# Kernel tuning notes

Hardware: AMD Instinct MI355X
Metric: run time of the kernel (lower is better)

## Reference

```python
import jax, jax.numpy as jnp
import numpy as np

G, N, D, L, T = 64, 64, 128, 4, 10
SLOPE = 0.01
BN_EPS = 1e-5


def _gin(x, adj, mask, W1, b1, W2, b2, eps):
    # x: [B,N,D], adj: [B,N,N], mask: [B,N] bool
    agg = jnp.einsum('bnm,bmd->bnd', adj, x)
    h = (1.0 + eps) * x + agg
    h = jax.nn.leaky_relu(h @ W1 + b1, SLOPE)
    h = h @ W2 + b2
    return h * mask[..., None].astype(h.dtype)


def _masked_bn(h, mask, gamma, beta):
    # training-mode BatchNorm1d over the masked (valid) rows only
    m = mask[..., None].astype(h.dtype)
    cnt = jnp.sum(m)
    mean = jnp.sum(h * m, axis=(0, 1)) / cnt
    var = jnp.sum(((h - mean) ** 2) * m, axis=(0, 1)) / cnt  # biased, as BN
    hn = (h - mean) * jax.lax.rsqrt(var + BN_EPS) * gamma + beta
    return jnp.where(mask[..., None], hn, h)


def _seg_mean(v, idx, num_segments):
    s = jax.ops.segment_sum(v, idx, num_segments=num_segments)
    c = jax.ops.segment_sum(jnp.ones((v.shape[0],), v.dtype), idx, num_segments=num_segments)
    return s / jnp.maximum(c, 1.0).reshape((num_segments,) + (1,) * (v.ndim - 1))


def setup_inputs() -> dict:
    key = jax.random.key(0)
    ks = jax.random.split(key, 16)
    S = G * N
    # original graphs: symmetric binary adjacency, no self loops
    a = (jax.random.uniform(ks[0], (G, N, N)) > 0.9).astype(jnp.float32)
    a = jnp.triu(a, 1)
    original_adj = a + a.transpose(0, 2, 1)
    original_mask = jnp.ones((G, N), dtype=bool)
    # node-deleted policy: subgraph s of graph s//N deletes node s%N
    graph_idx = jnp.repeat(jnp.arange(G), N)
    deleted = jnp.tile(jnp.arange(N), G)
    mask = jnp.ones((S, N), dtype=bool).at[jnp.arange(S), deleted].set(False)
    mf = mask.astype(jnp.float32)
    adj = original_adj[graph_idx] * mf[:, :, None] * mf[:, None, :]
    x = jax.random.normal(ks[1], (S, N, D), dtype=jnp.float32)
    sc = 1.0 / np.sqrt(D)
    inp = dict(
        x=x, adj=adj, original_adj=original_adj,
        gnn_W1=jax.random.normal(ks[2], (L, D, D)) * sc,
        gnn_b1=jnp.zeros((L, D)),
        gnn_W2=jax.random.normal(ks[3], (L, D, D)) * sc,
        gnn_b2=jnp.zeros((L, D)),
        gnn_eps=jnp.zeros((L,)),
        gs_W1=jax.random.normal(ks[4], (L, D, D)) * sc,
        gs_b1=jnp.zeros((L, D)),
        gs_W2=jax.random.normal(ks[5], (L, D, D)) * sc,
        gs_b2=jnp.zeros((L, D)),
        gs_eps=jnp.zeros((L,)),
        bn_gamma=jnp.ones((L, D)), bn_beta=jnp.zeros((L, D)),
        bns_gamma=jnp.ones((L, D)), bns_beta=jnp.zeros((L, D)),
        fin_W1=jax.random.normal(ks[6], (D, 2 * D)) * sc,
        fin_b1=jnp.zeros((2 * D,)),
        fin_W2=jax.random.normal(ks[7], (2 * D, T)) * (1.0 / np.sqrt(2 * D)),
        fin_b2=jnp.zeros((T,)),
        mask=mask, original_mask=original_mask, graph_idx=graph_idx,
    )
    return inp


def reference(x, adj, original_adj, gnn_W1, gnn_b1, gnn_W2, gnn_b2, gnn_eps,
              gs_W1, gs_b1, gs_W2, gs_b2, gs_eps,
              bn_gamma, bn_beta, bns_gamma, bns_beta,
              fin_W1, fin_b1, fin_W2, fin_b2,
              mask, original_mask, graph_idx):
    for i in range(L):
        h1 = _gin(x, adj, mask, gnn_W1[i], gnn_b1[i], gnn_W2[i], gnn_b2[i], gnn_eps[i])
        h1 = _masked_bn(h1, mask, bn_gamma[i], bn_beta[i])
        x_sum = _seg_mean(x, graph_idx, G)  # [G,N,D] scatter-mean over subgraphs
        h2 = _gin(x_sum, original_adj, original_mask, gs_W1[i], gs_b1[i], gs_W2[i], gs_b2[i], gs_eps[i])
        h2 = _masked_bn(h2, original_mask, bns_gamma[i], bns_beta[i])
        x = jax.nn.leaky_relu(h1 + h2[graph_idx], SLOPE)
    num_nodes = jnp.sum(mask, axis=-1).astype(x.dtype)  # [S]
    h_sub = jnp.sum(x, axis=1) / num_nodes[:, None]     # mean pool per subgraph
    h_graph = _seg_mean(h_sub, graph_idx, G)            # [G,D]
    out = jax.nn.leaky_relu(h_graph @ fin_W1 + fin_b1, SLOPE) @ fin_W2 + fin_b2
    return out
```

## Files before the change

### kernel.cpp

```cpp
#include <hip/hip_runtime.h>
#include <hip/hip_bf16.h>


typedef __bf16 bf16x8 __attribute__((ext_vector_type(8)));
typedef float f32x4 __attribute__((ext_vector_type(4)));
typedef unsigned short us8 __attribute__((ext_vector_type(8)));
typedef unsigned short us4 __attribute__((ext_vector_type(4)));
typedef unsigned u32x4 __attribute__((ext_vector_type(4)));
typedef unsigned u32x2 __attribute__((ext_vector_type(2)));

__device__ __forceinline__ unsigned short f2b(float f) {
  unsigned u = __builtin_bit_cast(unsigned, f);
  u += 0x7FFFu + ((u >> 16) & 1u);
  return (unsigned short)(u >> 16);
}
__device__ __forceinline__ unsigned cvtpk(float lo, float hi) {
  unsigned r;
  asm("v_cvt_pk_bf16_f32 %0, %1, %2" : "=v"(r) : "v"(lo), "v"(hi));
  return r;
}
__device__ __forceinline__ float b2f(unsigned short h) {
  return __builtin_bit_cast(float, (unsigned)h << 16);
}
__device__ __forceinline__ f32x4 mm(bf16x8 a, bf16x8 b, f32x4 c) {
  return __builtin_amdgcn_mfma_f32_16x16x32_bf16(a, b, c, 0, 0, 0);
}
__device__ __forceinline__ bf16x8 frag(const char* base, int row, int Kelems, int k0) {
  int off = (row * Kelems + k0) * 2;
  off ^= (row & 7) << 4;
  return *(const bf16x8*)(base + off);
}
__device__ __forceinline__ float lk(float v) { return fmaxf(v, 0.01f * v); }

__global__ __launch_bounds__(256) void k_prep(const float* __restrict__ g1,
    const float* __restrict__ g2, const float* __restrict__ s1,
    const float* __restrict__ s2, unsigned short* __restrict__ wt) {
  int b = blockIdx.x;
  int l = b >> 2, j = b & 3;
  const float* src = (j == 0 ? g1 : j == 1 ? g2 : j == 2 ? s1 : s2) + l * 16384;
  unsigned short* dst = wt + b * 16384;
  for (int e = threadIdx.x; e < 16384; e += 256) {
    int n = e >> 7, k = e & 127;
    dst[e] = f2b(src[k * 128 + n]);
  }
}

__global__ __launch_bounds__(256) void k_pack(const float* __restrict__ adj,
    const float* __restrict__ oadj, unsigned short* __restrict__ badj,
    unsigned short* __restrict__ boadj) {
  int bid = blockIdx.x, t = threadIdx.x;
  bool SUB = bid < 4096;
  int sub = SUB ? bid : bid - 4096;
  const float* src = SUB ? adj : oadj;
  unsigned short* dst = SUB ? badj : boadj;
  const float* p = src + (size_t)sub * 4096 + (t >> 2) * 64 + (t & 3) * 16;
  unsigned bits = 0;
  #pragma unroll
  for (int j4 = 0; j4 < 4; ++j4) {
    float4 v = *(const float4*)(p + j4 * 4);
    bits |= (unsigned)(v.x != 0.f) << (j4 * 4);
    bits |= (unsigned)(v.y != 0.f) << (j4 * 4 + 1);
    bits |= (unsigned)(v.z != 0.f) << (j4 * 4 + 2);
    bits |= (unsigned)(v.w != 0.f) << (j4 * 4 + 3);
  }
  dst[(size_t)sub * 256 + t] = (unsigned short)bits;
}

__global__ __launch_bounds__(256) void k_castseg(const float* __restrict__ x,
    unsigned short* __restrict__ xw, float* __restrict__ pxs) {
  int b2 = blockIdx.x, bb = b2 >> 2, c = b2 & 3, t = threadIdx.x;
  int e0 = c * 2048 + t * 8;
  float acc[8];
  #pragma unroll
  for (int j = 0; j < 8; ++j) acc[j] = 0.f;
  for (int ss = 0; ss < 16; ++ss) {
    size_t sb = ((size_t)bb * 16 + ss) * 8192 + e0;
    float4 v0 = *(const float4*)(x + sb);
    float4 v1 = *(const float4*)(x + sb + 4);
    acc[0] += v0.x; acc[1] += v0.y; acc[2] += v0.z; acc[3] += v0.w;
    acc[4] += v1.x; acc[5] += v1.y; acc[6] += v1.z; acc[7] += v1.w;
    u32x4 pk;
    pk.x = cvtpk(v0.x, v0.y); pk.y = cvtpk(v0.z, v0.w);
    pk.z = cvtpk(v1.x, v1.y); pk.w = cvtpk(v1.z, v1.w);
    *(us8*)(xw + sb) = __builtin_bit_cast(us8, pk);
  }
  float* o = pxs + (size_t)bb * 8192 + e0;
  *(float4*)o = make_float4(acc[0], acc[1], acc[2], acc[3]);
  *(float4*)(o + 4) = make_float4(acc[4], acc[5], acc[6], acc[7]);
}

template<int LAST>
__global__ __launch_bounds__(256) void k_xpart(const unsigned short* __restrict__ h1T,
    const unsigned short* __restrict__ h2T, const float* __restrict__ bnA,
    const float* __restrict__ bnB, const float* __restrict__ bnsA,
    const float* __restrict__ bnsB, float* __restrict__ pxsT,
    float* __restrict__ ppool) {
  int b2 = blockIdx.x, bb = b2 >> 2, c = b2 & 3, g = bb >> 2;
  int t = threadIdx.x;
  int d = c * 32 + (t >> 3), n0 = (t & 7) * 8;
  size_t off = (size_t)d * 64 + n0;
  float A1 = bnA[d], B1 = bnB[d];
  float A2 = bnsA[d], B2 = bnsB[d];
  float hb[8];
  {
    us8 v = *(const us8*)(h2T + (size_t)g * 8192 + off);
    #pragma unroll
    for (int j = 0; j < 8; ++j) hb[j] = fmaf(b2f(v[j]), A2, B2);
  }
  float acc[8];
  #pragma unroll
  for (int j = 0; j < 8; ++j) acc[j] = 0.f;
  for (int ss = 0; ss < 16; ++ss) {
    int s = bb * 16 + ss;
    int del = s & 63;
    us8 a = *(const us8*)(h1T + (size_t)s * 8192 + off);
    #pragma unroll
    for (int j = 0; j < 8; ++j) {
      float hv = ((n0 + j) != del) ? fmaf(b2f(a[j]), A1, B1) : 0.f;
      acc[j] += lk(hv + hb[j]);
    }
  }
  if (!LAST) {
    float* o = pxsT + (size_t)bb * 8192 + off;
    *(float4*)o       = make_float4(acc[0], acc[1], acc[2], acc[3]);
    *(float4*)(o + 4) = make_float4(acc[4], acc[5], acc[6], acc[7]);
  } else {
    float s8 = ((acc[0] + acc[1]) + (acc[2] + acc[3])) + ((acc[4] + acc[5]) + (acc[6] + acc[7]));
    s8 += __shfl_xor(s8, 1, 64);
    s8 += __shfl_xor(s8, 2, 64);
    s8 += __shfl_xor(s8, 4, 64);
    if ((t & 7) == 0) ppool[(size_t)bb * 128 + d] = s8;
  }
}

template<int FIRST>
__global__ __launch_bounds__(512, 4) void k_gin(
    const unsigned short* __restrict__ xw, unsigned short* __restrict__ h1T,
    const unsigned short* __restrict__ h2prev, unsigned short* __restrict__ h2out,
    const float* __restrict__ pxs,
    const unsigned short* __restrict__ badj, const unsigned short* __restrict__ boadj,
    const unsigned short* __restrict__ W1g, const unsigned short* __restrict__ W2g,
    const unsigned short* __restrict__ W1s, const unsigned short* __restrict__ W2s,
    const float* __restrict__ b1g, const float* __restrict__ b2g,
    const float* __restrict__ b1s, const float* __restrict__ b2s,
    const float* __restrict__ epg, const float* __restrict__ epss,
    const float* __restrict__ bnA, const float* __restrict__ bnB,
    const float* __restrict__ bnsA, const float* __restrict__ bnsB,
    float* __restrict__ p1s, float* __restrict__ p1q,
    float* __restrict__ p2s, float* __restrict__ p2q) {
  __shared__ __align__(16) char lds[40960];
  char* ldsAdj = lds;
  char* ldsB   = lds + 8192;
  char* ldsC   = lds + 24576;

  const int tid = threadIdx.x;
  const int bid = blockIdx.x;
  const bool SUB = bid < 4096;
  const int lb = SUB ? bid : bid - 4096;
  const int wv = tid >> 6, ln = tid & 63;
  const int lr = ln & 15, lkh = ln >> 4;
  const int wrow = wv * 16 + lr;
  const float ep1 = 1.0f + (SUB ? epg[0] : epss[0]);
  const int del = SUB ? (bid & 63) : -1;
  const unsigned short* W1t = SUB ? W1g : W1s;
  const unsigned short* W2t = SUB ? W2g : W2s;

  bf16x8 w1f[4], w2f[4];
  #pragma unroll
  for (int kk = 0; kk < 4; ++kk) {
    w1f[kk] = *(const bf16x8*)(W1t + (size_t)wrow * 128 + kk * 32 + lkh * 8);
    w2f[kk] = *(const bf16x8*)(W2t + (size_t)wrow * 128 + kk * 32 + lkh * 8);
  }
  const float bb1 = (SUB ? b1g : b1s)[wrow];
  const float bb2 = (SUB ? b2g : b2s)[wrow];

  {
    const unsigned char* bits =
        (const unsigned char*)(SUB ? badj + (size_t)lb * 256 : boadj + (size_t)lb * 256);
    unsigned char bbt = bits[tid];
    int row = tid >> 3, o = tid & 7;
    unsigned short ep1b = f2b(ep1);
    us8 v;
    #pragma unroll
    for (int j = 0; j < 8; ++j) v[j] = ((bbt >> j) & 1) ? (unsigned short)0x3F80 : (unsigned short)0;
    int j0 = row - o * 8;
    if (j0 >= 0 && j0 < 8) v[j0] = ep1b;
    int e = tid * 8;
    *(us8*)(ldsAdj + ((e << 1) ^ ((row & 7) << 4))) = v;
  }
  if (FIRST) {
    if (SUB) {
      const unsigned short* xg = xw + (size_t)bid * 8192;
      for (int e = tid * 8; e < 8192; e += 4096)
        *(us8*)(ldsC + e * 2) = *(const us8*)(xg + e);
    } else {
      const float* p = pxs + (size_t)lb * 4 * 8192;
      int e0 = tid * 16;
      #pragma unroll
      for (int cc = 0; cc < 4; ++cc) {
        float4 s = {0.f, 0.f, 0.f, 0.f};
        #pragma unroll
        for (int qt = 0; qt < 4; ++qt) {
          float4 v = *(const float4*)(p + qt * 8192 + e0 + cc * 4);
          s.x += v.x; s.y += v.y; s.z += v.z; s.w += v.w;
        }
        u32x2 pk;
        pk.x = cvtpk(s.x * 0.015625f, s.y * 0.015625f);
        pk.y = cvtpk(s.z * 0.015625f, s.w * 0.015625f);
        *(us4*)(ldsC + (e0 + cc * 4) * 2) = __builtin_bit_cast(us4, pk);
      }
    }
    __syncthreads();
    int d = tid & 127, mg = (tid >> 7) * 16;
    #pragma unroll
    for (int mb = 0; mb < 16; mb += 8) {
      us8 v;
      #pragma unroll
      for (int j = 0; j < 8; ++j)
        v[j] = *(const unsigned short*)(ldsC + ((mg + mb + j) << 8) + (d << 1));
      *(us8*)(ldsB + (((d << 7) + ((mg + mb) << 1)) ^ ((d & 7) << 4))) = v;
    }
  } else {
    int d = tid >> 2, n0 = (tid & 3) * 16;
    if (SUB) {
      const unsigned short* h1g = h1T + (size_t)bid * 8192 + d * 64 + n0;
      const unsigned short* h2g = h2prev + (size_t)(bid >> 6) * 8192 + d * 64 + n0;
      float A1 = bnA[d], B1 = bnB[d];
      float A2 = bnsA[d], B2 = bnsB[d];
      #pragma unroll
      for (int cc = 0; cc < 2; ++cc) {
        us8 a = *(const us8*)(h1g + cc * 8);
        us8 b = *(const us8*)(h2g + cc * 8);
        float xv[8];
        #pragma unroll
        for (int j = 0; j < 8; ++j) {
          int m = n0 + cc * 8 + j;
          float hv = (m != del) ? fmaf(b2f(a[j]), A1, B1) : 0.f;
          xv[j] = lk(hv + fmaf(b2f(b[j]), A2, B2));
        }
        u32x4 pk;
        pk.x = cvtpk(xv[0], xv[1]); pk.y = cvtpk(xv[2], xv[3]);
        pk.z = cvtpk(xv[4], xv[5]); pk.w = cvtpk(xv[6], xv[7]);
        *(us8*)(ldsB + (((d * 64 + n0 + cc * 8) * 2) ^ ((d & 7) << 4))) = __builtin_bit_cast(us8, pk);
      }
    } else {
      const float* p = pxs + (size_t)lb * 4 * 8192 + d * 64 + n0;
      #pragma unroll
      for (int cc = 0; cc < 4; ++cc) {
        float4 s = {0.f, 0.f, 0.f, 0.f};
        #pragma unroll
        for (int qt = 0; qt < 4; ++qt) {
          float4 v = *(const float4*)(p + qt * 8192 + cc * 4);
          s.x += v.x; s.y += v.y; s.z += v.z; s.w += v.w;
        }
        u32x2 pk;
        pk.x = cvtpk(s.x * 0.015625f, s.y * 0.015625f);
        pk.y = cvtpk(s.z * 0.015625f, s.w * 0.015625f);
        *(us4*)(ldsB + (((d * 64 + n0 + cc * 4) * 2) ^ ((d & 7) << 4))) = __builtin_bit_cast(us4, pk);
      }
    }
  }
  __syncthreads();

  {
    f32x4 acc[4] = {};
    #pragma unroll
    for (int rt = 0; rt < 4; ++rt) {
      #pragma unroll
      for (int k0 = 0; k0 < 64; k0 += 32) {
        bf16x8 a = frag(ldsAdj, rt * 16 + lr, 64, k0 + lkh * 8);
        bf16x8 b = frag(ldsB, wrow, 64, k0 + lkh * 8);
        acc[rt] = mm(a, b, acc[rt]);
      }
    }
    #pragma unroll
    for (int rt = 0; rt < 4; ++rt) {
      unsigned p01 = cvtpk(acc[rt][0], acc[rt][1]);
      unsigned p23 = cvtpk(acc[rt][2], acc[rt][3]);
      int r0 = rt * 16 + lkh * 4;
      *(unsigned short*)(ldsC + ((((r0 + 0) << 8) + (wrow << 1)) ^ (((r0 + 0) & 7) << 4))) = (unsigned short)p01;
      *(unsigned short*)(ldsC + ((((r0 + 1) << 8) + (wrow << 1)) ^ (((r0 + 1) & 7) << 4))) = (unsigned short)(p01 >> 16);
      *(unsigned short*)(ldsC + ((((r0 + 2) << 8) + (wrow << 1)) ^ (((r0 + 2) & 7) << 4))) = (unsigned short)p23;
      *(unsigned short*)(ldsC + ((((r0 + 3) << 8) + (wrow << 1)) ^ (((r0 + 3) & 7) << 4))) = (unsigned short)(p23 >> 16);
    }
  }
  __syncthreads();

  #pragma unroll
  for (int rt = 0; rt < 4; ++rt) {
    f32x4 acc = {};
    #pragma unroll
    for (int kk = 0; kk < 4; ++kk) {
      bf16x8 a = frag(ldsC, rt * 16 + lr, 128, kk * 32 + lkh * 8);
      acc = mm(a, w1f[kk], acc);
    }
    float u0 = lk(acc[0] + bb1), u1 = lk(acc[1] + bb1);
    float u2 = lk(acc[2] + bb1), u3 = lk(acc[3] + bb1);
    unsigned p01 = cvtpk(u0, u1);
    unsigned p23 = cvtpk(u2, u3);
    int r0 = rt * 16 + lkh * 4;
    *(unsigned short*)(ldsB + ((((r0 + 0) << 8) + (wrow << 1)) ^ (((r0 + 0) & 7) << 4))) = (unsigned short)p01;
    *(unsigned short*)(ldsB + ((((r0 + 1) << 8) + (wrow << 1)) ^ (((r0 + 1) & 7) << 4))) = (unsigned short)(p01 >> 16);
    *(unsigned short*)(ldsB + ((((r0 + 2) << 8) + (wrow << 1)) ^ (((r0 + 2) & 7) << 4))) = (unsigned short)p23;
    *(unsigned short*)(ldsB + ((((r0 + 3) << 8) + (wrow << 1)) ^ (((r0 + 3) & 7) << 4))) = (unsigned short)(p23 >> 16);
  }
  __syncthreads();

  {
    float sm = 0.f, sq = 0.f;
    #pragma unroll
    for (int rt = 0; rt < 4; ++rt) {
      f32x4 acc = {};
      #pragma unroll
      for (int kk = 0; kk < 4; ++kk) {
        bf16x8 a = frag(ldsB, rt * 16 + lr, 128, kk * 32 + lkh * 8);
        acc = mm(a, w2f[kk], acc);
      }
      float v0 = acc[0] + bb2, v1 = acc[1] + bb2, v2 = acc[2] + bb2, v3 = acc[3] + bb2;
      int m0 = rt * 16 + lkh * 4;
      if (m0 + 0 == del) v0 = 0.f;
      if (m0 + 1 == del) v1 = 0.f;
      if (m0 + 2 == del) v2 = 0.f;
      if (m0 + 3 == del) v3 = 0.f;
      sm += v0 + v1 + v2 + v3;
      sq += v0 * v0 + v1 * v1 + v2 * v2 + v3 * v3;
      u32x2 pk;
      pk.x = cvtpk(v0, v1);
      pk.y = cvtpk(v2, v3);
      *(us4*)(ldsC + (((wrow * 64 + m0) * 2) ^ ((wrow & 7) << 4))) = __builtin_bit_cast(us4, pk);
    }
    sm += __shfl_xor(sm, 16, 64); sm += __shfl_xor(sm, 32, 64);
    sq += __shfl_xor(sq, 16, 64); sq += __shfl_xor(sq, 32, 64);
    if (ln < 16) {
      float* ps = SUB ? p1s + (size_t)bid * 128 : p2s + (size_t)lb * 128;
      float* pq = SUB ? p1q + (size_t)bid * 128 : p2q + (size_t)lb * 128;
      ps[wrow] = sm;
      pq[wrow] = sq;
    }
  }
  __syncthreads();

  unsigned short* hout = SUB ? h1T + (size_t)bid * 8192 : h2out + (size_t)lb * 8192;
  {
    int e0 = tid * 16;
    int d = e0 >> 6;
    *(us8*)(hout + e0)     = *(const us8*)(ldsC + (((e0)     * 2) ^ ((d & 7) << 4)));
    *(us8*)(hout + e0 + 8) = *(const us8*)(ldsC + (((e0 + 8) * 2) ^ ((d & 7) << 4)));
  }
}

__global__ __launch_bounds__(256) void k_bnred(const float* __restrict__ p1s,
    const float* __restrict__ p1q, float* __restrict__ q1s, float* __restrict__ q1q) {
  __shared__ float red[512];
  int b = blockIdx.x, tid = threadIdx.x;
  int d = tid & 127, jh = tid >> 7;
  float s = 0.f, q = 0.f;
  for (int j = b * 64 + jh; j < b * 64 + 64; j += 2) {
    s += p1s[(size_t)j * 128 + d];
    q += p1q[(size_t)j * 128 + d];
  }
  red[tid] = s; red[256 + tid] = q;
  __syncthreads();
  if (tid < 128) {
    q1s[(size_t)b * 128 + d] = red[d] + red[d + 128];
    q1q[(size_t)b * 128 + d] = red[256 + d] + red[384 + d];
  }
}

__global__ __launch_bounds__(128) void k_bnfin(const float* __restrict__ q1s,
    const float* __restrict__ q1q, const float* __restrict__ p2s,
    const float* __restrict__ p2q, const float* __restrict__ gam1,
    const float* __restrict__ bet1, const float* __restrict__ gam2,
    const float* __restrict__ bet2, float* __restrict__ bnA, float* __restrict__ bnB,
    float* __restrict__ bnsA, float* __restrict__ bnsB) {
  int d = threadIdx.x;
  float s = 0.f, q = 0.f, s2 = 0.f, q2 = 0.f;
  for (int j = 0; j < 64; ++j) {
    s  += q1s[j * 128 + d];  q  += q1q[j * 128 + d];
    s2 += p2s[j * 128 + d];  q2 += p2q[j * 128 + d];
  }
  const float cnt1 = 4096.0f * 63.0f;
  float mean = s / cnt1;
  float var = q / cnt1 - mean * mean;
  float A = gam1[d] * rsqrtf(var + 1e-5f);
  bnA[d] = A; bnB[d] = bet1[d] - mean * A;
  float mean2 = s2 / 4096.0f;
  float var2 = q2 / 4096.0f - mean2 * mean2;
  float A2 = gam2[d] * rsqrtf(var2 + 1e-5f);
  bnsA[d] = A2; bnsB[d] = bet2[d] - mean2 * A2;
}

__global__ __launch_bounds__(256) void k_final(const float* __restrict__ ppool,
    const float* __restrict__ W1, const float* __restrict__ b1,
    const float* __restrict__ W2, const float* __restrict__ b2,
    float* __restrict__ out) {
  __shared__ float hg[128];
  __shared__ float z[256];
  int g = blockIdx.x, t = threadIdx.x;
  if (t < 128) {
    float s = ppool[(size_t)(g * 4 + 0) * 128 + t] + ppool[(size_t)(g * 4 + 1) * 128 + t]
            + ppool[(size_t)(g * 4 + 2) * 128 + t] + ppool[(size_t)(g * 4 + 3) * 128 + t];
    hg[t] = s * (1.0f / (63.0f * 64.0f));
  }
  __syncthreads();
  float a = b1[t];
  for (int d = 0; d < 128; ++d) a = fmaf(hg[d], W1[d * 256 + t], a);
  z[t] = lk(a);
  __syncthreads();
  if (t < 10) {
    float o = b2[t];
    for (int j = 0; j < 256; ++j) o = fmaf(z[j], W2[j * 10 + t], o);
    out[g * 10 + t] = o;
  }
}

extern "C" void kernel_launch(void* const* d_in, const int* in_sizes, int n_in,
                              void* d_out, int out_size, void* d_ws, size_t ws_size,
                              hipStream_t stream) {
  (void)in_sizes; (void)n_in; (void)out_size; (void)ws_size;
  const float* x    = (const float*)d_in[0];
  const float* adj  = (const float*)d_in[1];
  const float* oadj = (const float*)d_in[2];
  const float* gW1  = (const float*)d_in[3];
  const float* gb1  = (const float*)d_in[4];
  const float* gW2  = (const float*)d_in[5];
  const float* gb2  = (const float*)d_in[6];
  const float* geps = (const float*)d_in[7];
  const float* sW1  = (const float*)d_in[8];
  const float* sb1  = (const float*)d_in[9];
  const float* sW2  = (const float*)d_in[10];
  const float* sb2  = (const float*)d_in[11];
  const float* seps = (const float*)d_in[12];
  const float* bng  = (const float*)d_in[13];
  const float* bnb  = (const float*)d_in[14];
  const float* bnsg = (const float*)d_in[15];
  const float* bnsb = (const float*)d_in[16];
  const float* fW1  = (const float*)d_in[17];
  const float* fb1  = (const float*)d_in[18];
  const float* fW2  = (const float*)d_in[19];
  const float* fb2  = (const float*)d_in[20];
  float* out = (float*)d_out;

  char* w = (char*)d_ws;
  unsigned short* xw   = (unsigned short*)w; w += 67108864;
  unsigned short* h1T  = (unsigned short*)w; w += 67108864;
  unsigned short* h2a  = (unsigned short*)w; w += 1048576;
  unsigned short* h2b  = (unsigned short*)w; w += 1048576;
  unsigned short* badj = (unsigned short*)w; w += 2097152;
  unsigned short* boadj= (unsigned short*)w; w += 32768;
  unsigned short* wt   = (unsigned short*)w; w += 524288;
  float* pxs  = (float*)w;          w += 8388608;
  float* p1s  = (float*)w;          w += 2097152;
  float* p1q  = (float*)w;          w += 2097152;
  float* p2s  = (float*)w;          w += 32768;
  float* p2q  = (float*)w;          w += 32768;
  float* q1s  = (float*)w;          w += 32768;
  float* q1q  = (float*)w;          w += 32768;
  float* bnA  = (float*)w;          w += 512;
  float* bnB  = (float*)w;          w += 512;
  float* bnsA = (float*)w;          w += 512;
  float* bnsB = (float*)w;          w += 512;
  float* ppool= (float*)w;          w += 131072;

  unsigned short* h2buf[2] = {h2a, h2b};

  k_prep<<<16, 256, 0, stream>>>(gW1, gW2, sW1, sW2, wt);
  k_pack<<<4160, 256, 0, stream>>>(adj, oadj, badj, boadj);
  k_castseg<<<1024, 256, 0, stream>>>(x, xw, pxs);

  for (int i = 0; i < 4; ++i) {
    unsigned short* h2prev = h2buf[(i + 1) & 1];
    unsigned short* h2cur  = h2buf[i & 1];
    if (i > 0)
      k_xpart<0><<<1024, 256, 0, stream>>>(h1T, h2prev, bnA, bnB, bnsA, bnsB, pxs, ppool);
    if (i == 0)
      k_gin<1><<<4160, 512, 0, stream>>>(xw, h1T, h2prev, h2cur, pxs, badj, boadj,
          wt + 0 * 16384, wt + 1 * 16384, wt + 2 * 16384, wt + 3 * 16384,
          gb1, gb2, sb1, sb2, geps, seps, bnA, bnB, bnsA, bnsB, p1s, p1q, p2s, p2q);
    else
      k_gin<0><<<4160, 512, 0, stream>>>(xw, h1T, h2prev, h2cur, pxs, badj, boadj,
          wt + (i * 4 + 0) * 16384, wt + (i * 4 + 1) * 16384,
          wt + (i * 4 + 2) * 16384, wt + (i * 4 + 3) * 16384,
          gb1 + i * 128, gb2 + i * 128, sb1 + i * 128, sb2 + i * 128,
          geps + i, seps + i, bnA, bnB, bnsA, bnsB, p1s, p1q, p2s, p2q);
    k_bnred<<<64, 256, 0, stream>>>(p1s, p1q, q1s, q1q);
    k_bnfin<<<1, 128, 0, stream>>>(q1s, q1q, p2s, p2q, bng + i * 128,
        bnb + i * 128, bnsg + i * 128, bnsb + i * 128, bnA, bnB, bnsA, bnsB);
  }
  k_xpart<1><<<1024, 256, 0, stream>>>(h1T, h2buf[1], bnA, bnB, bnsA, bnsB, pxs, ppool);
  k_final<<<64, 256, 0, stream>>>(ppool, fW1, fb1, fW2, fb2, out);
}
```

Measured before the change: 420.8 us.

## Merge preprocessing kernels, raise MFMA wave priority, widen BN reductions

Merges the adjacency bit-packing and the x cast/segment-sum kernels into one launch, which removes a kernel launch and lets the two independent jobs overlap on the device. Wraps the MFMA loops in the GIN kernel with s_setprio so matrix-issuing waves get scheduling priority. Splits the BN partial reduction over twice as many blocks and gives the final BN kernel 256 threads with a shared-memory combine, shortening the serial reduction chains. The changes are small tail-latency tweaks, and the priority hint may have no effect or could perturb scheduling.

```diff
diff --git a/kernel.cpp b/kernel.cpp
--- a/kernel.cpp
+++ b/kernel.cpp
@@ -45,48 +45,49 @@
   }
 }
 
-__global__ __launch_bounds__(256) void k_pack(const float* __restrict__ adj,
-    const float* __restrict__ oadj, unsigned short* __restrict__ badj,
-    unsigned short* __restrict__ boadj) {
+__global__ __launch_bounds__(256) void k_pre(const float* __restrict__ adj,
+    const float* __restrict__ oadj, const float* __restrict__ x,
+    unsigned short* __restrict__ badj, unsigned short* __restrict__ boadj,
+    unsigned short* __restrict__ xw, float* __restrict__ pxs) {
   int bid = blockIdx.x, t = threadIdx.x;
-  bool SUB = bid < 4096;
-  int sub = SUB ? bid : bid - 4096;
-  const float* src = SUB ? adj : oadj;
-  unsigned short* dst = SUB ? badj : boadj;
-  const float* p = src + (size_t)sub * 4096 + (t >> 2) * 64 + (t & 3) * 16;
-  unsigned bits = 0;
-  #pragma unroll
-  for (int j4 = 0; j4 < 4; ++j4) {
-    float4 v = *(const float4*)(p + j4 * 4);
-    bits |= (unsigned)(v.x != 0.f) << (j4 * 4);
-    bits |= (unsigned)(v.y != 0.f) << (j4 * 4 + 1);
-    bits |= (unsigned)(v.z != 0.f) << (j4 * 4 + 2);
-    bits |= (unsigned)(v.w != 0.f) << (j4 * 4 + 3);
-  }
-  dst[(size_t)sub * 256 + t] = (unsigned short)bits;
-}
-
-__global__ __launch_bounds__(256) void k_castseg(const float* __restrict__ x,
-    unsigned short* __restrict__ xw, float* __restrict__ pxs) {
-  int b2 = blockIdx.x, bb = b2 >> 2, c = b2 & 3, t = threadIdx.x;
-  int e0 = c * 2048 + t * 8;
-  float acc[8];
-  #pragma unroll
-  for (int j = 0; j < 8; ++j) acc[j] = 0.f;
-  for (int ss = 0; ss < 16; ++ss) {
-    size_t sb = ((size_t)bb * 16 + ss) * 8192 + e0;
-    float4 v0 = *(const float4*)(x + sb);
-    float4 v1 = *(const float4*)(x + sb + 4);
-    acc[0] += v0.x; acc[1] += v0.y; acc[2] += v0.z; acc[3] += v0.w;
-    acc[4] += v1.x; acc[5] += v1.y; acc[6] += v1.z; acc[7] += v1.w;
-    u32x4 pk;
-    pk.x = cvtpk(v0.x, v0.y); pk.y = cvtpk(v0.z, v0.w);
-    pk.z = cvtpk(v1.x, v1.y); pk.w = cvtpk(v1.z, v1.w);
-    *(us8*)(xw + sb) = __builtin_bit_cast(us8, pk);
-  }
-  float* o = pxs + (size_t)bb * 8192 + e0;
-  *(float4*)o = make_float4(acc[0], acc[1], acc[2], acc[3]);
-  *(float4*)(o + 4) = make_float4(acc[4], acc[5], acc[6], acc[7]);
+  if (bid < 4160) {
+    bool SUB = bid < 4096;
+    int sub = SUB ? bid : bid - 4096;
+    const float* src = SUB ? adj : oadj;
+    unsigned short* dst = SUB ? badj : boadj;
+    const float* p = src + (size_t)sub * 4096 + (t >> 2) * 64 + (t & 3) * 16;
+    unsigned bits = 0;
+    #pragma unroll
+    for (int j4 = 0; j4 < 4; ++j4) {
+      float4 v = *(const float4*)(p + j4 * 4);
+      bits |= (unsigned)(v.x != 0.f) << (j4 * 4);
+      bits |= (unsigned)(v.y != 0.f) << (j4 * 4 + 1);
+      bits |= (unsigned)(v.z != 0.f) << (j4 * 4 + 2);
+      bits |= (unsigned)(v.w != 0.f) << (j4 * 4 + 3);
+    }
+    dst[(size_t)sub * 256 + t] = (unsigned short)bits;
+  } else {
+    int b2 = bid - 4160;
+    int bb = b2 >> 2, c = b2 & 3;
+    int e0 = c * 2048 + t * 8;
+    float acc[8];
+    #pragma unroll
+    for (int j = 0; j < 8; ++j) acc[j] = 0.f;
+    for (int ss = 0; ss < 16; ++ss) {
+      size_t sb = ((size_t)bb * 16 + ss) * 8192 + e0;
+      float4 v0 = *(const float4*)(x + sb);
+      float4 v1 = *(const float4*)(x + sb + 4);
+      acc[0] += v0.x; acc[1] += v0.y; acc[2] += v0.z; acc[3] += v0.w;
+      acc[4] += v1.x; acc[5] += v1.y; acc[6] += v1.z; acc[7] += v1.w;
+      u32x4 pk;
+      pk.x = cvtpk(v0.x, v0.y); pk.y = cvtpk(v0.z, v0.w);
+      pk.z = cvtpk(v1.x, v1.y); pk.w = cvtpk(v1.z, v1.w);
+      *(us8*)(xw + sb) = __builtin_bit_cast(us8, pk);
+    }
+    float* o = pxs + (size_t)bb * 8192 + e0;
+    *(float4*)o = make_float4(acc[0], acc[1], acc[2], acc[3]);
+    *(float4*)(o + 4) = make_float4(acc[4], acc[5], acc[6], acc[7]);
+  }
 }
 
 template<int LAST>
@@ -264,6 +265,7 @@
 
   {
     f32x4 acc[4] = {};
+    __builtin_amdgcn_s_setprio(1);
     #pragma unroll
     for (int rt = 0; rt < 4; ++rt) {
       #pragma unroll
@@ -273,6 +275,7 @@
         acc[rt] = mm(a, b, acc[rt]);
       }
     }
+    __builtin_amdgcn_s_setprio(0);
     #pragma unroll
     for (int rt = 0; rt < 4; ++rt) {
       unsigned p01 = cvtpk(acc[rt][0], acc[rt][1]);
@@ -289,11 +292,13 @@
   #pragma unroll
   for (int rt = 0; rt < 4; ++rt) {
     f32x4 acc = {};
+    __builtin_amdgcn_s_setprio(1);
     #pragma unroll
     for (int kk = 0; kk < 4; ++kk) {
       bf16x8 a = frag(ldsC, rt * 16 + lr, 128, kk * 32 + lkh * 8);
       acc = mm(a, w1f[kk], acc);
     }
+    __builtin_amdgcn_s_setprio(0);
     float u0 = lk(acc[0] + bb1), u1 = lk(acc[1] + bb1);
     float u2 = lk(acc[2] + bb1), u3 = lk(acc[3] + bb1);
     unsigned p01 = cvtpk(u0, u1);
@@ -311,11 +316,13 @@
     #pragma unroll
     for (int rt = 0; rt < 4; ++rt) {
       f32x4 acc = {};
+      __builtin_amdgcn_s_setprio(1);
       #pragma unroll
       for (int kk = 0; kk < 4; ++kk) {
         bf16x8 a = frag(ldsB, rt * 16 + lr, 128, kk * 32 + lkh * 8);
         acc = mm(a, w2f[kk], acc);
       }
+      __builtin_amdgcn_s_setprio(0);
       float v0 = acc[0] + bb2, v1 = acc[1] + bb2, v2 = acc[2] + bb2, v3 = acc[3] + bb2;
       int m0 = rt * 16 + lkh * 4;
       if (m0 + 0 == del) v0 = 0.f;
@@ -355,7 +362,7 @@
   int b = blockIdx.x, tid = threadIdx.x;
   int d = tid & 127, jh = tid >> 7;
   float s = 0.f, q = 0.f;
-  for (int j = b * 64 + jh; j < b * 64 + 64; j += 2) {
+  for (int j = b * 32 + jh; j < b * 32 + 32; j += 2) {
     s += p1s[(size_t)j * 128 + d];
     q += p1q[(size_t)j * 128 + d];
   }
@@ -367,27 +374,35 @@
   }
 }
 
-__global__ __launch_bounds__(128) void k_bnfin(const float* __restrict__ q1s,
+__global__ __launch_bounds__(256) void k_bnfin(const float* __restrict__ q1s,
     const float* __restrict__ q1q, const float* __restrict__ p2s,
     const float* __restrict__ p2q, const float* __restrict__ gam1,
     const float* __restrict__ bet1, const float* __restrict__ gam2,
     const float* __restrict__ bet2, float* __restrict__ bnA, float* __restrict__ bnB,
     float* __restrict__ bnsA, float* __restrict__ bnsB) {
-  int d = threadIdx.x;
+  __shared__ float sh[512];
+  int t = threadIdx.x, d = t & 127, half = t >> 7;
   float s = 0.f, q = 0.f, s2 = 0.f, q2 = 0.f;
-  for (int j = 0; j < 64; ++j) {
-    s  += q1s[j * 128 + d];  q  += q1q[j * 128 + d];
-    s2 += p2s[j * 128 + d];  q2 += p2q[j * 128 + d];
-  }
-  const float cnt1 = 4096.0f * 63.0f;
-  float mean = s / cnt1;
-  float var = q / cnt1 - mean * mean;
-  float A = gam1[d] * rsqrtf(var + 1e-5f);
-  bnA[d] = A; bnB[d] = bet1[d] - mean * A;
-  float mean2 = s2 / 4096.0f;
-  float var2 = q2 / 4096.0f - mean2 * mean2;
-  float A2 = gam2[d] * rsqrtf(var2 + 1e-5f);
-  bnsA[d] = A2; bnsB[d] = bet2[d] - mean2 * A2;
+  for (int j = half * 64; j < half * 64 + 64; ++j) {
+    s += q1s[j * 128 + d];  q += q1q[j * 128 + d];
+  }
+  for (int j = half * 32; j < half * 32 + 32; ++j) {
+    s2 += p2s[j * 128 + d]; q2 += p2q[j * 128 + d];
+  }
+  if (half) { sh[d] = s; sh[128 + d] = q; sh[256 + d] = s2; sh[384 + d] = q2; }
+  __syncthreads();
+  if (!half) {
+    s += sh[d]; q += sh[128 + d]; s2 += sh[256 + d]; q2 += sh[384 + d];
+    const float cnt1 = 4096.0f * 63.0f;
+    float mean = s / cnt1;
+    float var = q / cnt1 - mean * mean;
+    float A = gam1[d] * rsqrtf(var + 1e-5f);
+    bnA[d] = A; bnB[d] = bet1[d] - mean * A;
+    float mean2 = s2 / 4096.0f;
+    float var2 = q2 / 4096.0f - mean2 * mean2;
+    float A2 = gam2[d] * rsqrtf(var2 + 1e-5f);
+    bnsA[d] = A2; bnsB[d] = bet2[d] - mean2 * A2;
+  }
 }
 
 __global__ __launch_bounds__(256) void k_final(const float* __restrict__ ppool,
@@ -454,8 +469,8 @@
   float* p1q  = (float*)w;          w += 2097152;
   float* p2s  = (float*)w;          w += 32768;
   float* p2q  = (float*)w;          w += 32768;
-  float* q1s  = (float*)w;          w += 32768;
-  float* q1q  = (float*)w;          w += 32768;
+  float* q1s  = (float*)w;          w += 65536;
+  float* q1q  = (float*)w;          w += 65536;
   float* bnA  = (float*)w;          w += 512;
   float* bnB  = (float*)w;          w += 512;
   float* bnsA = (float*)w;          w += 512;
@@ -465,8 +480,7 @@
   unsigned short* h2buf[2] = {h2a, h2b};
 
   k_prep<<<16, 256, 0, stream>>>(gW1, gW2, sW1, sW2, wt);
-  k_pack<<<4160, 256, 0, stream>>>(adj, oadj, badj, boadj);
-  k_castseg<<<1024, 256, 0, stream>>>(x, xw, pxs);
+  k_pre<<<5184, 256, 0, stream>>>(adj, oadj, x, badj, boadj, xw, pxs);
 
   for (int i = 0; i < 4; ++i) {
     unsigned short* h2prev = h2buf[(i + 1) & 1];
@@ -483,8 +497,8 @@
           wt + (i * 4 + 2) * 16384, wt + (i * 4 + 3) * 16384,
           gb1 + i * 128, gb2 + i * 128, sb1 + i * 128, sb2 + i * 128,
           geps + i, seps + i, bnA, bnB, bnsA, bnsB, p1s, p1q, p2s, p2q);
-    k_bnred<<<64, 256, 0, stream>>>(p1s, p1q, q1s, q1q);
-    k_bnfin<<<1, 128, 0, stream>>>(q1s, q1q, p2s, p2q, bng + i * 128,
+    k_bnred<<<128, 256, 0, stream>>>(p1s, p1q, q1s, q1q);
+    k_bnfin<<<1, 256, 0, stream>>>(q1s, q1q, p2s, p2q, bng + i * 128,
         bnb + i * 128, bnsg + i * 128, bnsb + i * 128, bnA, bnB, bnsA, bnsB);
   }
   k_xpart<1><<<1024, 256, 0, stream>>>(h1T, h2buf[1], bnA, bnB, bnsA, bnsB, pxs, ppool);
```

Result: slower. 458.0 us (+8.8%).
